# Optimization experiments

Hardware: AMD Instinct MI355X
Metric: run time of the kernel (lower is better)

## Reference

```python
import jax, jax.numpy as jnp
import numpy as np
import math

B, N, M = 128, 32, 64           # batch, num_agents, num_other
OBS, ACT = 128, 16              # obs_input_dim, num_actions
D_QK = 128                      # obs_output_dim (== obs_output_dim_other)
D_AV = 64                       # obs_act_output_dim (== other)
F_IN = OBS + ACT                # obs_act_input_dim = 144


def _xavier(key, shape):
    fan_in, fan_out = shape[0], shape[1]
    limit = math.sqrt(6.0 / (fan_in + fan_out))
    return jax.random.uniform(key, shape, jnp.float32, -limit, limit)


def setup_inputs() -> dict:
    key = jax.random.key(0)
    ks = jax.random.split(key, 13)
    return {
        "states": jax.random.normal(ks[0], (B, N, OBS), jnp.float32),
        "policies": jax.random.uniform(ks[1], (B, N, ACT), jnp.float32),
        "actions": jax.random.uniform(ks[2], (B, N, ACT), jnp.float32),
        "states_other": jax.random.normal(ks[3], (B, M, OBS), jnp.float32),
        "actions_other": jax.random.uniform(ks[4], (B, M, ACT), jnp.float32),
        # weights stored as [in, out] (x @ W == nn.Linear without bias)
        "W_key": _xavier(ks[5], (OBS, D_QK)),
        "W_query": _xavier(ks[6], (OBS, D_QK)),
        "W_av": _xavier(ks[7], (F_IN, D_AV)),
        "W_key_other": _xavier(ks[8], (OBS, D_QK)),
        "W_query_other": _xavier(ks[9], (OBS, D_QK)),
        "W_av_other": _xavier(ks[10], (F_IN, D_AV)),
        "W_f1": _xavier(ks[11], (2 * D_AV, 64)),
        "W_f2": _xavier(ks[12], (64, 1)),
    }


def reference(states, policies, actions, states_other, actions_other,
              W_key, W_query, W_av, W_key_other, W_query_other,
              W_av_other, W_f1, W_f2):
    b, n, _ = states.shape
    obs_actions = jnp.concatenate([states, actions], axis=-1)   # [B,N,F_IN]
    obs_policy = jnp.concatenate([states, policies], axis=-1)   # [B,N,F_IN]

    key_obs = states @ W_key                                    # [B,N,D_QK]
    query_obs = states @ W_query                                # [B,N,D_QK]
    d_k = W_key.shape[1]
    weight = jax.nn.softmax(
        jnp.einsum('bid,bjd->bij', query_obs, key_obs) / math.sqrt(d_k), axis=-1)
    ret_weight = weight

    # place_policies is identity on (j,k): oap[b,j,k] = obs_policy[b,k] if j==k else obs_actions[b,k]
    eye = jnp.eye(n, dtype=states.dtype)[None, :, :, None]       # [1,N,N,1]
    oap = eye * obs_policy[:, None, :, :] + (1.0 - eye) * obs_actions[:, None, :, :]
    attention_values = jnp.tanh(oap @ W_av)                      # [B,N,N,D_AV] (j,k)

    # repeat-mul-sum == weighted reduction over k: wav[b,i,j,d] = sum_k w[b,i,k] av[b,j,k,d]
    wav = jnp.einsum('bik,bjkd->bijd', weight, attention_values)  # [B,N,N,D_AV]

    obs_actions_other = jnp.concatenate([states_other, actions_other], axis=-1)
    keys_other = states_other @ W_key_other                      # [B,M,D_QK]
    query_agent = states @ W_query_other                         # [B,N,D_QK]
    av_other = jnp.tanh(obs_actions_other @ W_av_other)          # [B,M,D_AV]
    d_k_o = W_key_other.shape[1]
    weight_other = jax.nn.softmax(
        jnp.einsum('bid,bmd->bim', query_agent, keys_other) / math.sqrt(d_k_o), axis=-1)
    wav_other = jnp.einsum('bim,bmd->bid', weight_other, av_other)  # [B,N,D_AV]

    # broadcast the per-agent other-branch features across the j axis for the concat
    wav_other_b = jnp.broadcast_to(wav_other[:, :, None, :], wav.shape[:-1] + (wav_other.shape[-1],))
    node_features = jnp.concatenate([wav, wav_other_b], axis=-1)  # [B,N,N,2*D_AV]

    h = jax.nn.leaky_relu(node_features @ W_f1, negative_slope=0.01)
    value = h @ W_f2                                              # [B,N,N,1]
    return value, ret_weight, weight_other
```

## Files before the change

### kernel.cpp

```cpp
#include <hip/hip_runtime.h>
#include <math.h>

#define WS_WQK   0
#define WS_WQKO  16384
#define WS_AVA   32768
#define WS_AVO   294912
#define WS_DPROJ 819200

#define INV_SQRT_DK 0.08838834764831845f

__device__ __forceinline__ float dot4(float4 a, float4 b) {
  return a.x*b.x + a.y*b.y + a.z*b.z + a.w*b.w;
}
__device__ __forceinline__ void fma4(float4& a, const float4 w, const float s) {
  a.x += w.x*s; a.y += w.y*s; a.z += w.z*s; a.w += w.w*s;
}

__global__ __launch_bounds__(256, 4) void k1_pre(
    const float* __restrict__ g_states, const float* __restrict__ g_pol,
    const float* __restrict__ g_act, const float* __restrict__ g_so,
    const float* __restrict__ g_ao,
    const float* __restrict__ Wq, const float* __restrict__ Wk,
    const float* __restrict__ Wqo, const float* __restrict__ Wko,
    const float* __restrict__ W_av, const float* __restrict__ W_avo,
    const float* __restrict__ W_f1, float* __restrict__ ws)
{
  __shared__ __align__(16) float pool[8448];
  const int t = threadIdx.x;
  int blk = blockIdx.x;

  if (blk < 32) {
    const float* A; const float* Bm; float* O;
    if (blk < 16) { A = Wq;  Bm = Wk;  O = ws + WS_WQK; }
    else          { A = Wqo; Bm = Wko; O = ws + WS_WQKO; blk -= 16; }
    const int tr = (blk >> 2) << 5;
    const int tc = (blk & 3) << 5;
    float* sA = pool;
    float* sB = pool + 4224;
    const float4* a4 = (const float4*)(A + tr * 128);
    const float4* b4 = (const float4*)(Bm + tc * 128);
    #pragma unroll
    for (int u = 0; u < 4; ++u) {
      int f = t + u * 256;
      int r = f >> 5, c4 = f & 31;
      *(float4*)(sA + r*132 + c4*4) = a4[f];
      *(float4*)(sB + r*132 + c4*4) = b4[f];
    }
    __syncthreads();
    const int e = t & 31, cl0 = t >> 5;
    float acc[4] = {0,0,0,0};
    #pragma unroll 4
    for (int d4 = 0; d4 < 32; ++d4) {
      float4 bv = *(const float4*)(sB + e*132 + d4*4);
      #pragma unroll
      for (int rr = 0; rr < 4; ++rr) {
        float4 av = *(const float4*)(sA + (cl0 + rr*8)*132 + d4*4);
        acc[rr] += dot4(av, bv);
      }
    }
    #pragma unroll
    for (int rr = 0; rr < 4; ++rr)
      O[(tr + cl0 + rr*8)*128 + tc + e] = acc[rr];
    return;
  }
  blk -= 32;

  if (blk < 256) {
    const int b  = blk >> 1;
    const int jh = blk & 1;
    float* s_pre = pool;
    float* s_dl  = pool + 2112;
    {
      const int wv_  = t >> 6;
      const int ap   = wv_ & 1;
      const int rq   = wv_ >> 1;
      const int lane = t & 63;
      const float* gs = g_states + b*4096 + (jh*16 + rq*8)*128;
      const float* gt = (ap ? g_pol : g_act) + b*512 + (jh*16 + rq*8)*16;
      float acc[8];
      #pragma unroll
      for (int r = 0; r < 8; ++r) acc[r] = 0.f;
      #pragma unroll 4
      for (int c4 = 0; c4 < 32; ++c4) {
        const float w0 = W_av[(c4*4+0)*64 + lane];
        const float w1 = W_av[(c4*4+1)*64 + lane];
        const float w2 = W_av[(c4*4+2)*64 + lane];
        const float w3 = W_av[(c4*4+3)*64 + lane];
        #pragma unroll
        for (int r = 0; r < 8; ++r) {
          float4 sv = *(const float4*)(gs + r*128 + c4*4);
          acc[r] += sv.x*w0 + sv.y*w1 + sv.z*w2 + sv.w*w3;
        }
      }
      #pragma unroll
      for (int c4 = 0; c4 < 4; ++c4) {
        const float w0 = W_av[(128 + c4*4+0)*64 + lane];
        const float w1 = W_av[(128 + c4*4+1)*64 + lane];
        const float w2 = W_av[(128 + c4*4+2)*64 + lane];
        const float w3 = W_av[(128 + c4*4+3)*64 + lane];
        #pragma unroll
        for (int r = 0; r < 8; ++r) {
          float4 sv = *(const float4*)(gt + r*16 + c4*4);
          acc[r] += sv.x*w0 + sv.y*w1 + sv.z*w2 + sv.w*w3;
        }
      }
      #pragma unroll
      for (int r = 0; r < 8; ++r)
        s_pre[(rq*8 + r)*132 + ap*64 + lane] = acc[r];
    }
    __syncthreads();
    {
      const int r = t >> 4, d0 = (t & 15) << 2;
      float4 a0 = *(const float4*)(s_pre + r*132 + d0);
      float4 p0 = *(const float4*)(s_pre + r*132 + 64 + d0);
      float4 va0, dl0;
      va0.x = tanhf(a0.x); va0.y = tanhf(a0.y); va0.z = tanhf(a0.z); va0.w = tanhf(a0.w);
      dl0.x = tanhf(p0.x) - va0.x; dl0.y = tanhf(p0.y) - va0.y;
      dl0.z = tanhf(p0.z) - va0.z; dl0.w = tanhf(p0.w) - va0.w;
      *(float4*)(ws + WS_AVA + b*2048 + (jh*16 + r)*64 + d0) = va0;
      *(float4*)(s_dl + r*68 + d0) = dl0;
    }
    __syncthreads();
    {
      const int h = t & 63;
      const int j0 = (t >> 6) << 2;
      float acc[4] = {0,0,0,0};
      #pragma unroll 4
      for (int d4 = 0; d4 < 16; ++d4) {
        float w0 = W_f1[(d4*4+0)*64 + h];
        float w1 = W_f1[(d4*4+1)*64 + h];
        float w2 = W_f1[(d4*4+2)*64 + h];
        float w3 = W_f1[(d4*4+3)*64 + h];
        #pragma unroll
        for (int q = 0; q < 4; ++q) {
          float4 dv = *(const float4*)(s_dl + (j0+q)*68 + d4*4);
          acc[q] += dv.x*w0 + dv.y*w1 + dv.z*w2 + dv.w*w3;
        }
      }
      #pragma unroll
      for (int q = 0; q < 4; ++q)
        ws[WS_DPROJ + b*2048 + (jh*16 + j0+q)*64 + h] = acc[q];
    }
    return;
  }
  blk -= 256;

  {
    const int b = blk >> 2, m0 = (blk & 3) << 4;
    const int wv_  = t >> 6;
    const int lane = t & 63;
    const float* gso = g_so + (b*64 + m0 + wv_*4) * 128;
    const float* gao = g_ao + (b*64 + m0 + wv_*4) * 16;
    float acc[4] = {0.f, 0.f, 0.f, 0.f};
    #pragma unroll 4
    for (int c4 = 0; c4 < 32; ++c4) {
      const float w0 = W_avo[(c4*4+0)*64 + lane];
      const float w1 = W_avo[(c4*4+1)*64 + lane];
      const float w2 = W_avo[(c4*4+2)*64 + lane];
      const float w3 = W_avo[(c4*4+3)*64 + lane];
      #pragma unroll
      for (int r = 0; r < 4; ++r) {
        float4 sv = *(const float4*)(gso + r*128 + c4*4);
        acc[r] += sv.x*w0 + sv.y*w1 + sv.z*w2 + sv.w*w3;
      }
    }
    #pragma unroll
    for (int c4 = 0; c4 < 4; ++c4) {
      const float w0 = W_avo[(128 + c4*4+0)*64 + lane];
      const float w1 = W_avo[(128 + c4*4+1)*64 + lane];
      const float w2 = W_avo[(128 + c4*4+2)*64 + lane];
      const float w3 = W_avo[(128 + c4*4+3)*64 + lane];
      #pragma unroll
      for (int r = 0; r < 4; ++r) {
        float4 sv = *(const float4*)(gao + r*16 + c4*4);
        acc[r] += sv.x*w0 + sv.y*w1 + sv.z*w2 + sv.w*w3;
      }
    }
    #pragma unroll
    for (int r = 0; r < 4; ++r)
      ws[WS_AVO + b*4096 + (m0 + wv_*4 + r)*64 + lane] = tanhf(acc[r]);
  }
}

__global__ __launch_bounds__(512, 4) void k2_main(
    const float* __restrict__ g_states, const float* __restrict__ g_so,
    const float* __restrict__ W_f1, const float* __restrict__ W_f2,
    const float* __restrict__ ws, float* __restrict__ out)
{
  __shared__ __align__(16) float pool[17472];
  float* s_st   = pool;
  float* s_red  = pool + 4352;
  float* s_avA  = pool + 4352;
  float* s_dp   = pool + 6528;
  float* s_avO  = pool;
  float* s_P    = pool + 12800;
  float* s_w    = pool + 14944;
  float* s_wo   = pool + 15232;
  float* s_S    = pool + 15776;
  float* s_wavo = pool + 16320;
  float* s_base = pool + 16864;
  float* s_wf2  = pool + 17408;

  const int t = threadIdx.x;
  const int b = blockIdx.x >> 2;
  const int i0 = (blockIdx.x & 3) << 3;

  {
    const float4* gs4 = (const float4*)(g_states + b * 4096);
    #pragma unroll
    for (int u = 0; u < 2; ++u) {
      int f = t + u * 512;
      int r = f >> 5, c4 = f & 31;
      *(float4*)(s_st + r*132 + c4*4) = gs4[f];
    }
    if (t < 16) *(float4*)(s_wf2 + t*4) = ((const float4*)W_f2)[t];
  }

  {
    const int wave = t >> 6;
    const int kc   = wave & 3;
    const int rh   = wave >> 2;
    const int col  = t & 63;
    const float* Wp = (col < 32) ? (ws + WS_WQK + col*4)
                                 : (ws + WS_WQKO + (col-32)*4);
    const float* srow = g_states + b*4096 + (i0 + rh*4)*128 + kc*32;
    float4 acc[4];
    #pragma unroll
    for (int r = 0; r < 4; ++r) acc[r] = make_float4(0.f,0.f,0.f,0.f);
    #pragma unroll 2
    for (int c4 = 0; c4 < 8; ++c4) {
      float4 sv[4];
      #pragma unroll
      for (int r = 0; r < 4; ++r)
        sv[r] = *(const float4*)(srow + r*128 + c4*4);
      #pragma unroll
      for (int k = 0; k < 4; ++k) {
        float4 wv = *(const float4*)(Wp + (kc*32 + c4*4 + k)*128);
        #pragma unroll
        for (int r = 0; r < 4; ++r)
          fma4(acc[r], wv, ((const float*)&sv[r])[k]);
      }
    }
    #pragma unroll
    for (int r = 0; r < 4; ++r)
      *(float4*)(s_red + ((kc*8 + rh*4 + r)*66 + col)*4) = acc[r];
  }
  __syncthreads();
  {
    const int r = t >> 6, col = t & 63;
    float4 a0 = *(const float4*)(s_red + ((0*8 + r)*66 + col)*4);
    float4 a1 = *(const float4*)(s_red + ((1*8 + r)*66 + col)*4);
    float4 a2 = *(const float4*)(s_red + ((2*8 + r)*66 + col)*4);
    float4 a3 = *(const float4*)(s_red + ((3*8 + r)*66 + col)*4);
    float4 s4;
    s4.x = (a0.x + a1.x) + (a2.x + a3.x);
    s4.y = (a0.y + a1.y) + (a2.y + a3.y);
    s4.z = (a0.z + a1.z) + (a2.z + a3.z);
    s4.w = (a0.w + a1.w) + (a2.w + a3.w);
    *(float4*)(s_P + r*268 + col*4) = s4;
  }
  __syncthreads();

  {
    const int r = t >> 6, j = t & 31, half = (t >> 5) & 1;
    const int e0 = half << 4;
    float acc = 0.f;
    #pragma unroll 8
    for (int e4 = 0; e4 < 16; ++e4) {
      float4 p4  = *(const float4*)(s_P + r*268 + (e0 + e4)*4);
      float4 st4 = *(const float4*)(s_st + j*132 + (e0 + e4)*4);
      acc += dot4(p4, st4);
    }
    acc += __shfl_xor(acc, 32, 64);
    acc *= INV_SQRT_DK;
    float mx = acc;
    for (int off = 16; off; off >>= 1) mx = fmaxf(mx, __shfl_xor(mx, off, 32));
    float ev = __expf(acc - mx);
    float sum = ev;
    for (int off = 16; off; off >>= 1) sum += __shfl_xor(sum, off, 32);
    float wn = ev / sum;
    if (half == 0) {
      out[131072 + b*1024 + (i0 + r)*32 + j] = wn;
      s_w[r*36 + j] = wn;
    }
  }
  __syncthreads();

  for (int tt = 0; tt < 2; ++tt) {
    const float4* gt4 = (const float4*)(g_so + (b*64 + tt*32) * 128);
    #pragma unroll
    for (int u = 0; u < 2; ++u) {
      int f = t + u * 512;
      int r = f >> 5, c4 = f & 31;
      *(float4*)(s_st + r*132 + c4*4) = gt4[f];
    }
    __syncthreads();
    const int r = t >> 6, m = t & 31, half = (t >> 5) & 1;
    const int c0 = half << 4;
    float acc = 0.f;
    #pragma unroll 8
    for (int c4 = 0; c4 < 16; ++c4) {
      float4 p4  = *(const float4*)(s_P + r*268 + 128 + (c0 + c4)*4);
      float4 st4 = *(const float4*)(s_st + m*132 + (c0 + c4)*4);
      acc += dot4(p4, st4);
    }
    acc += __shfl_xor(acc, 32, 64);
    if (half == 0) s_wo[r*68 + tt*32 + m] = acc * INV_SQRT_DK;
    __syncthreads();
  }

  {
    const int r = t >> 6, l = t & 63;
    float v = s_wo[r*68 + l];
    float mx = v;
    for (int off = 32; off; off >>= 1) mx = fmaxf(mx, __shfl_xor(mx, off, 64));
    float ev = __expf(v - mx);
    float sum = ev;
    for (int off = 32; off; off >>= 1) sum += __shfl_xor(sum, off, 64);
    float wn = ev / sum;
    out[262144 + b*2048 + (i0 + r)*64 + l] = wn;
    s_wo[r*68 + l] = wn;
  }
  {
    int f = t;
    int k = f >> 4, dq = f & 15;
    *(float4*)(s_avA + k*68 + dq*4) = ((const float4*)(ws + WS_AVA + b*2048))[f];
    *(float4*)(s_dp  + k*68 + dq*4) = ((const float4*)(ws + WS_DPROJ + b*2048))[f];
  }
  #pragma unroll
  for (int u = 0; u < 2; ++u) {
    int f = t + u * 512;
    int m = f >> 4, dq = f & 15;
    *(float4*)(s_avO + m*68 + dq*4) = ((const float4*)(ws + WS_AVO + b*4096))[f];
  }
  __syncthreads();

  if (t < 128) {
    const int i = t >> 4, dq = (t & 15) << 2;
    float4 acc = {0,0,0,0};
    #pragma unroll 4
    for (int k = 0; k < 32; ++k) {
      float4 a4 = *(const float4*)(s_avA + k*68 + dq);
      float wv = s_w[i*36 + k];
      acc.x += wv*a4.x; acc.y += wv*a4.y; acc.z += wv*a4.z; acc.w += wv*a4.w;
    }
    *(float4*)(s_S + i*68 + dq) = acc;
  } else if (t < 384) {
    const int tt2 = t - 128;
    const int mh = tt2 >> 7;
    const int i = (tt2 & 127) >> 4, dq = (tt2 & 15) << 2;
    float4 acc = {0,0,0,0};
    #pragma unroll 4
    for (int mm = 0; mm < 32; ++mm) {
      const int m = mh*32 + mm;
      float4 a4 = *(const float4*)(s_avO + m*68 + dq);
      float wv = s_wo[i*68 + m];
      acc.x += wv*a4.x; acc.y += wv*a4.y; acc.z += wv*a4.z; acc.w += wv*a4.w;
    }
    float* dst = mh ? (s_P + i*68 + dq) : (s_wavo + i*68 + dq);
    *(float4*)dst = acc;
  }
  __syncthreads();

  {
    const int h = t & 63, i = t >> 6;
    float a0 = 0.f;
    #pragma unroll 4
    for (int d = 0; d < 64; ++d) {
      float w1v = W_f1[d*64 + h];
      float w2v = W_f1[(64 + d)*64 + h];
      a0 += s_S[i*68 + d]*w1v + (s_wavo[i*68 + d] + s_P[i*68 + d])*w2v;
    }
    s_base[i*68 + h] = a0;
  }
  __syncthreads();

  {
    const int i = t >> 6, j = t & 31, half = (t >> 5) & 1;
    const float wij = s_w[i*36 + j];
    float acc = 0.f;
    #pragma unroll 4
    for (int hq = half*8; hq < half*8 + 8; ++hq) {
      float4 b4 = *(const float4*)(s_base + i*68 + hq*4);
      float4 d4 = *(const float4*)(s_dp + j*68 + hq*4);
      float4 f4 = *(const float4*)(s_wf2 + hq*4);
      float p0 = b4.x + wij*d4.x; p0 = p0 > 0.f ? p0 : 0.01f*p0;
      float p1 = b4.y + wij*d4.y; p1 = p1 > 0.f ? p1 : 0.01f*p1;
      float p2 = b4.z + wij*d4.z; p2 = p2 > 0.f ? p2 : 0.01f*p2;
      float p3 = b4.w + wij*d4.w; p3 = p3 > 0.f ? p3 : 0.01f*p3;
      acc += p0*f4.x + p1*f4.y + p2*f4.z + p3*f4.w;
    }
    acc += __shfl_xor(acc, 32, 64);
    if (half == 0)
      out[b*1024 + (i0 + i)*32 + j] = acc;
  }
}

extern "C" void kernel_launch(void* const* d_in, const int* in_sizes, int n_in,
                              void* d_out, int out_size, void* d_ws, size_t ws_size,
                              hipStream_t stream) {
  const float* states        = (const float*)d_in[0];
  const float* policies      = (const float*)d_in[1];
  const float* actions       = (const float*)d_in[2];
  const float* states_other  = (const float*)d_in[3];
  const float* actions_other = (const float*)d_in[4];
  const float* W_key         = (const float*)d_in[5];
  const float* W_query       = (const float*)d_in[6];
  const float* W_av          = (const float*)d_in[7];
  const float* W_key_other   = (const float*)d_in[8];
  const float* W_query_other = (const float*)d_in[9];
  const float* W_av_other    = (const float*)d_in[10];
  const float* W_f1          = (const float*)d_in[11];
  const float* W_f2          = (const float*)d_in[12];
  float* out = (float*)d_out;
  float* ws  = (float*)d_ws;

  k1_pre<<<800, 256, 0, stream>>>(states, policies, actions, states_other,
                                  actions_other, W_query, W_key,
                                  W_query_other, W_key_other, W_av, W_av_other,
                                  W_f1, ws);
  k2_main<<<512, 512, 0, stream>>>(states, states_other, W_f1, W_f2, ws, out);
}
```

Baseline: 138.6 us.

## Stage activations in LDS and enlarge per-block tiles in pre-pass kernel

The attention-value and delta-projection blocks in k1_pre now handle a full batch (32 rows) instead of half, and the other-branch blocks handle 32 rows instead of 16. In both cases the states and action/policy rows are first staged into shared memory, so each thread reuses more weight loads across rows. This cuts the grid from 800 to 416 blocks and lowers the occupancy hint. k2_main now reads states from the already-loaded shared copy instead of global memory, with an added barrier. The cost is fewer blocks, more registers per thread and larger LDS use.

```diff
diff --git a/kernel.cpp b/kernel.cpp
--- a/kernel.cpp
+++ b/kernel.cpp
@@ -16,7 +16,7 @@
   a.x += w.x*s; a.y += w.y*s; a.z += w.z*s; a.w += w.w*s;
 }
 
-__global__ __launch_bounds__(256, 4) void k1_pre(
+__global__ __launch_bounds__(256, 2) void k1_pre(
     const float* __restrict__ g_states, const float* __restrict__ g_pol,
     const float* __restrict__ g_act, const float* __restrict__ g_so,
     const float* __restrict__ g_ao,
@@ -25,7 +25,7 @@
     const float* __restrict__ W_av, const float* __restrict__ W_avo,
     const float* __restrict__ W_f1, float* __restrict__ ws)
 {
-  __shared__ __align__(16) float pool[8448];
+  __shared__ __align__(16) float pool[11904];
   const int t = threadIdx.x;
   int blk = blockIdx.x;
 
@@ -65,21 +65,40 @@
   }
   blk -= 32;
 
-  if (blk < 256) {
-    const int b  = blk >> 1;
-    const int jh = blk & 1;
-    float* s_pre = pool;
-    float* s_dl  = pool + 2112;
+  if (blk < 128) {
+    const int b = blk;
+    float* s_in  = pool;
+    float* s_t   = pool + 4224;
+    float* s_pre = pool + 5504;
+    float* s_dl  = pool + 9728;
+    {
+      const float4* gs4 = (const float4*)(g_states + b*4096);
+      #pragma unroll
+      for (int u = 0; u < 4; ++u) {
+        int f = t + u * 256;
+        int r = f >> 5, c4 = f & 31;
+        *(float4*)(s_in + r*132 + c4*4) = gs4[f];
+      }
+      if (t < 128) {
+        int r = t >> 2, c4 = t & 3;
+        *(float4*)(s_t + r*40 + c4*4) = ((const float4*)(g_act + b*512))[t];
+      } else {
+        int t2 = t - 128;
+        int r = t2 >> 2, c4 = t2 & 3;
+        *(float4*)(s_t + r*40 + 20 + c4*4) = ((const float4*)(g_pol + b*512))[t2];
+      }
+    }
+    __syncthreads();
     {
       const int wv_  = t >> 6;
       const int ap   = wv_ & 1;
-      const int rq   = wv_ >> 1;
+      const int rh   = wv_ >> 1;
       const int lane = t & 63;
-      const float* gs = g_states + b*4096 + (jh*16 + rq*8)*128;
-      const float* gt = (ap ? g_pol : g_act) + b*512 + (jh*16 + rq*8)*16;
-      float acc[8];
-      #pragma unroll
-      for (int r = 0; r < 8; ++r) acc[r] = 0.f;
+      const float* s_rows = s_in + rh*16*132;
+      const float* s_tl   = s_t + rh*16*40 + ap*20;
+      float acc[16];
+      #pragma unroll
+      for (int r = 0; r < 16; ++r) acc[r] = 0.f;
       #pragma unroll 4
       for (int c4 = 0; c4 < 32; ++c4) {
         const float w0 = W_av[(c4*4+0)*64 + lane];
@@ -87,8 +106,8 @@
         const float w2 = W_av[(c4*4+2)*64 + lane];
         const float w3 = W_av[(c4*4+3)*64 + lane];
         #pragma unroll
-        for (int r = 0; r < 8; ++r) {
-          float4 sv = *(const float4*)(gs + r*128 + c4*4);
+        for (int r = 0; r < 16; ++r) {
+          float4 sv = *(const float4*)(s_rows + r*132 + c4*4);
           acc[r] += sv.x*w0 + sv.y*w1 + sv.z*w2 + sv.w*w3;
         }
       }
@@ -99,32 +118,39 @@
         const float w2 = W_av[(128 + c4*4+2)*64 + lane];
         const float w3 = W_av[(128 + c4*4+3)*64 + lane];
         #pragma unroll
-        for (int r = 0; r < 8; ++r) {
-          float4 sv = *(const float4*)(gt + r*16 + c4*4);
+        for (int r = 0; r < 16; ++r) {
+          float4 sv = *(const float4*)(s_tl + r*40 + c4*4);
           acc[r] += sv.x*w0 + sv.y*w1 + sv.z*w2 + sv.w*w3;
         }
       }
       #pragma unroll
-      for (int r = 0; r < 8; ++r)
-        s_pre[(rq*8 + r)*132 + ap*64 + lane] = acc[r];
+      for (int r = 0; r < 16; ++r)
+        s_pre[(rh*16 + r)*132 + ap*64 + lane] = acc[r];
     }
     __syncthreads();
     {
-      const int r = t >> 4, d0 = (t & 15) << 2;
+      const int r = t >> 3, d0 = (t & 7) << 3;
       float4 a0 = *(const float4*)(s_pre + r*132 + d0);
+      float4 a1 = *(const float4*)(s_pre + r*132 + d0 + 4);
       float4 p0 = *(const float4*)(s_pre + r*132 + 64 + d0);
-      float4 va0, dl0;
+      float4 p1 = *(const float4*)(s_pre + r*132 + 64 + d0 + 4);
+      float4 va0, va1, dl0, dl1;
       va0.x = tanhf(a0.x); va0.y = tanhf(a0.y); va0.z = tanhf(a0.z); va0.w = tanhf(a0.w);
+      va1.x = tanhf(a1.x); va1.y = tanhf(a1.y); va1.z = tanhf(a1.z); va1.w = tanhf(a1.w);
       dl0.x = tanhf(p0.x) - va0.x; dl0.y = tanhf(p0.y) - va0.y;
       dl0.z = tanhf(p0.z) - va0.z; dl0.w = tanhf(p0.w) - va0.w;
-      *(float4*)(ws + WS_AVA + b*2048 + (jh*16 + r)*64 + d0) = va0;
-      *(float4*)(s_dl + r*68 + d0) = dl0;
+      dl1.x = tanhf(p1.x) - va1.x; dl1.y = tanhf(p1.y) - va1.y;
+      dl1.z = tanhf(p1.z) - va1.z; dl1.w = tanhf(p1.w) - va1.w;
+      *(float4*)(ws + WS_AVA + b*2048 + r*64 + d0)     = va0;
+      *(float4*)(ws + WS_AVA + b*2048 + r*64 + d0 + 4) = va1;
+      *(float4*)(s_dl + r*68 + d0)     = dl0;
+      *(float4*)(s_dl + r*68 + d0 + 4) = dl1;
     }
     __syncthreads();
     {
       const int h = t & 63;
-      const int j0 = (t >> 6) << 2;
-      float acc[4] = {0,0,0,0};
+      const int j0 = (t >> 6) << 3;
+      float acc[8] = {0,0,0,0,0,0,0,0};
       #pragma unroll 4
       for (int d4 = 0; d4 < 16; ++d4) {
         float w0 = W_f1[(d4*4+0)*64 + h];
@@ -132,26 +158,44 @@
         float w2 = W_f1[(d4*4+2)*64 + h];
         float w3 = W_f1[(d4*4+3)*64 + h];
         #pragma unroll
-        for (int q = 0; q < 4; ++q) {
+        for (int q = 0; q < 8; ++q) {
           float4 dv = *(const float4*)(s_dl + (j0+q)*68 + d4*4);
           acc[q] += dv.x*w0 + dv.y*w1 + dv.z*w2 + dv.w*w3;
         }
       }
       #pragma unroll
-      for (int q = 0; q < 4; ++q)
-        ws[WS_DPROJ + b*2048 + (jh*16 + j0+q)*64 + h] = acc[q];
+      for (int q = 0; q < 8; ++q)
+        ws[WS_DPROJ + b*2048 + (j0+q)*64 + h] = acc[q];
     }
     return;
   }
-  blk -= 256;
-
-  {
-    const int b = blk >> 2, m0 = (blk & 3) << 4;
+  blk -= 128;
+
+  {
+    const int b = blk >> 1, m0 = (blk & 1) << 5;
+    float* s_so = pool;
+    float* s_ao = pool + 4224;
+    {
+      const float4* gso4 = (const float4*)(g_so + (b*64 + m0) * 128);
+      #pragma unroll
+      for (int u = 0; u < 4; ++u) {
+        int f = t + u * 256;
+        int r = f >> 5, c4 = f & 31;
+        *(float4*)(s_so + r*132 + c4*4) = gso4[f];
+      }
+      if (t < 128) {
+        int r = t >> 2, c4 = t & 3;
+        *(float4*)(s_ao + r*20 + c4*4) = ((const float4*)(g_ao + (b*64 + m0)*16))[t];
+      }
+    }
+    __syncthreads();
     const int wv_  = t >> 6;
     const int lane = t & 63;
-    const float* gso = g_so + (b*64 + m0 + wv_*4) * 128;
-    const float* gao = g_ao + (b*64 + m0 + wv_*4) * 16;
-    float acc[4] = {0.f, 0.f, 0.f, 0.f};
+    const float* s_rows = s_so + wv_*8*132;
+    const float* s_tl   = s_ao + wv_*8*20;
+    float acc[8];
+    #pragma unroll
+    for (int r = 0; r < 8; ++r) acc[r] = 0.f;
     #pragma unroll 4
     for (int c4 = 0; c4 < 32; ++c4) {
       const float w0 = W_avo[(c4*4+0)*64 + lane];
@@ -159,8 +203,8 @@
       const float w2 = W_avo[(c4*4+2)*64 + lane];
       const float w3 = W_avo[(c4*4+3)*64 + lane];
       #pragma unroll
-      for (int r = 0; r < 4; ++r) {
-        float4 sv = *(const float4*)(gso + r*128 + c4*4);
+      for (int r = 0; r < 8; ++r) {
+        float4 sv = *(const float4*)(s_rows + r*132 + c4*4);
         acc[r] += sv.x*w0 + sv.y*w1 + sv.z*w2 + sv.w*w3;
       }
     }
@@ -171,14 +215,14 @@
       const float w2 = W_avo[(128 + c4*4+2)*64 + lane];
       const float w3 = W_avo[(128 + c4*4+3)*64 + lane];
       #pragma unroll
-      for (int r = 0; r < 4; ++r) {
-        float4 sv = *(const float4*)(gao + r*16 + c4*4);
+      for (int r = 0; r < 8; ++r) {
+        float4 sv = *(const float4*)(s_tl + r*20 + c4*4);
         acc[r] += sv.x*w0 + sv.y*w1 + sv.z*w2 + sv.w*w3;
       }
     }
     #pragma unroll
-    for (int r = 0; r < 4; ++r)
-      ws[WS_AVO + b*4096 + (m0 + wv_*4 + r)*64 + lane] = tanhf(acc[r]);
+    for (int r = 0; r < 8; ++r)
+      ws[WS_AVO + b*4096 + (m0 + wv_*8 + r)*64 + lane] = tanhf(acc[r]);
   }
 }
 
@@ -215,6 +259,7 @@
     }
     if (t < 16) *(float4*)(s_wf2 + t*4) = ((const float4*)W_f2)[t];
   }
+  __syncthreads();
 
   {
     const int wave = t >> 6;
@@ -223,7 +268,7 @@
     const int col  = t & 63;
     const float* Wp = (col < 32) ? (ws + WS_WQK + col*4)
                                  : (ws + WS_WQKO + (col-32)*4);
-    const float* srow = g_states + b*4096 + (i0 + rh*4)*128 + kc*32;
+    const float* srow = s_st + (i0 + rh*4)*132 + kc*32;
     float4 acc[4];
     #pragma unroll
     for (int r = 0; r < 4; ++r) acc[r] = make_float4(0.f,0.f,0.f,0.f);
@@ -232,7 +277,7 @@
       float4 sv[4];
       #pragma unroll
       for (int r = 0; r < 4; ++r)
-        sv[r] = *(const float4*)(srow + r*128 + c4*4);
+        sv[r] = *(const float4*)(srow + r*132 + c4*4);
       #pragma unroll
       for (int k = 0; k < 4; ++k) {
         float4 wv = *(const float4*)(Wp + (kc*32 + c4*4 + k)*128);
@@ -415,7 +460,7 @@
   float* out = (float*)d_out;
   float* ws  = (float*)d_ws;
 
-  k1_pre<<<800, 256, 0, stream>>>(states, policies, actions, states_other,
+  k1_pre<<<416, 256, 0, stream>>>(states, policies, actions, states_other,
                                   actions_other, W_query, W_key,
                                   W_query_other, W_key_other, W_av, W_av_other,
                                   W_f1, ws);
```

Measured after the change: 128.1 us. 7.5% less time.
